# Kernel optimization log

Hardware: AMD Instinct MI355X
Metric: run time of the kernel (lower is better)

Reference implementation:

```python
import jax, jax.numpy as jnp
import numpy as np
from functools import partial

B, F, H, G, S = 8192, 16, 128, 4, 20  # batch, features, hidden, goals, SUBSTEPS
A_IZH, B_IZH, C_IZH, D_IZH = 0.02, 0.2, -65.0, 8.0  # Izhikevich 'RS' params
RATE_DECAY = 0.9
GAMMA, LR = 0.95, 1e-3


def izh_step(v, u, rate, I):
    """One Izhikevich substep (dt=1): returns new (v, u, rate, spike)."""
    v_new = v + (0.04 * v * v + 5.0 * v + 140.0 - u + I)
    u_new = u + A_IZH * (B_IZH * v - u)
    spike = (v_new >= 30.0).astype(v.dtype)
    v_new = jnp.where(spike > 0, C_IZH, v_new)
    u_new = u_new + spike * D_IZH
    rate_new = RATE_DECAY * rate + (1.0 - RATE_DECAY) * spike
    return v_new, u_new, rate_new, spike


def build_features(energy, threat, food_visible, goal, cls_probs, DA_, NA_):
    # [B,16] = [4 scalars | one-hot goal (4) | cls_probs (5) | DA | NA | hunger]
    base = jnp.stack([energy / 100.0, threat, food_visible, 1.0 - energy / 100.0], axis=-1)
    onehot = jax.nn.one_hot(goal, G, dtype=base.dtype)
    tail = jnp.stack([DA_, NA_, jnp.maximum(0.0, 0.5 - energy / 100.0)], axis=-1)
    return jnp.concatenate([base, onehot, cls_probs, tail], axis=-1)


def setup_inputs() -> dict:
    key = jax.random.key(0)
    ks = jax.random.split(key, 16)
    energy = jax.random.uniform(ks[0], (B,)) * 100.0
    threat = jax.random.uniform(ks[1], (B,))
    food_visible = jax.random.uniform(ks[2], (B,))
    goal = jax.random.randint(ks[3], (B,), 0, G)
    prev_goal = jax.random.randint(ks[4], (B,), 0, G)
    DA_ = jax.random.uniform(ks[5], (B,))
    NA_ = jax.random.uniform(ks[6], (B,))
    reward = jax.random.normal(ks[7], (B,)) * 0.5
    cls_probs = jax.nn.softmax(jax.random.normal(ks[8], (B, 5)), axis=-1)
    a_in = 0.5 * np.sqrt(6.0 / (F + H))   # xavier_uniform gain 0.5
    a_out = 0.3 * np.sqrt(6.0 / (H + G))  # xavier_uniform gain 0.3
    W_in_w = jax.random.uniform(ks[9], (B, H, F), minval=-a_in, maxval=a_in)
    W_in_b = jax.random.uniform(ks[10], (B, H), minval=-1.0, maxval=1.0) / np.sqrt(F)
    W_out_w = jax.random.uniform(ks[11], (B, G, H), minval=-a_out, maxval=a_out)
    W_out_b = jax.random.uniform(ks[12], (B, G), minval=-1.0, maxval=1.0) / np.sqrt(H)
    hv = jnp.full((B, H), -65.0)
    hu = B_IZH * hv
    hrate = jnp.zeros((B, H))
    vv = jnp.full((B, G), -65.0)
    vu = B_IZH * vv
    vrate = jnp.zeros((B, G))
    elig_in = jnp.zeros((B, H, F))
    elig_out = jnp.zeros((B, G, H))
    prev_values = jnp.zeros((B, G))
    prev_features = jax.random.uniform(ks[13], (B, F))
    noise = jax.random.normal(ks[14], (S, B, H))
    return dict(energy=energy, threat=threat, food_visible=food_visible, goal=goal,
                prev_goal=prev_goal, DA_=DA_, NA_=NA_, reward=reward, cls_probs=cls_probs,
                W_in_w=W_in_w, W_in_b=W_in_b, W_out_w=W_out_w, W_out_b=W_out_b,
                hv=hv, hu=hu, hrate=hrate, vv=vv, vu=vu, vrate=vrate,
                elig_in=elig_in, elig_out=elig_out, prev_values=prev_values,
                prev_features=prev_features, noise=noise)


def reference(energy, threat, food_visible, goal, prev_goal, DA_, NA_, reward, cls_probs,
              W_in_w, W_in_b, W_out_w, W_out_b, hv, hu, hrate, vv, vu, vrate,
              elig_in, elig_out, prev_values, prev_features, noise):
    features = build_features(energy, threat, food_visible, goal, cls_probs, DA_, NA_)  # [B,F]
    I_in = jnp.einsum('bhf,bf->bh', W_in_w, features) + W_in_b
    I_in = I_in * (5.0 / (jnp.mean(jnp.abs(I_in), axis=-1, keepdims=True) + 1e-8))

    def step(carry, nz):
        hv, hu, hrate, vv, vu, vrate, hsp, vsp = carry
        hv, hu, hrate, sp_h = izh_step(hv, hu, hrate, I_in + 0.3 * nz)
        I_out = jnp.einsum('bgh,bh->bg', W_out_w, hrate) + W_out_b
        I_out = I_out * (4.0 / (jnp.mean(jnp.abs(I_out), axis=-1, keepdims=True) + 1e-8))
        vv, vu, vrate, sp_v = izh_step(vv, vu, vrate, I_out)
        return (hv, hu, hrate, vv, vu, vrate, hsp + sp_h, vsp + sp_v), None

    carry0 = (hv, hu, hrate, vv, vu, vrate, jnp.zeros_like(hrate), jnp.zeros_like(vrate))
    (hv, hu, hrate, vv, vu, vrate, h_spikes, v_spikes), _ = jax.lax.scan(step, carry0, noise)

    values = jnp.einsum('bgh,bh->bg', W_out_w, hrate) + W_out_b  # [B,G]
    V_now = jnp.take_along_axis(values, goal[:, None], axis=1)[:, 0]
    V_prev = jnp.take_along_axis(prev_values, prev_goal[:, None], axis=1)[:, 0]
    td = reward + GAMMA * V_now - V_prev  # [B]

    elig_in_new = 0.9 * elig_in + hrate[:, :, None] * prev_features[:, None, :]
    elig_out_new = 0.9 * elig_out + vrate[:, :, None] * hrate[:, None, :]

    upd = (jnp.abs(td) > 1e-3)  # [B]
    scale = (LR * td * DA_)[:, None, None]
    W_in_new = jnp.where(upd[:, None, None], jnp.clip(W_in_w + scale * elig_in_new, -3.0, 3.0), W_in_w)
    W_out_new = jnp.where(upd[:, None, None], jnp.clip(W_out_w + scale * elig_out_new, -3.0, 3.0), W_out_w)

    hidden_active = jnp.mean((h_spikes > 0).astype(values.dtype), axis=-1)  # [B]
    return values, td, hidden_active, W_in_new, W_out_new, elig_in_new, elig_out_new
```

## Files before the change

### kernel.cpp

```cpp
#include <hip/hip_runtime.h>


namespace {

constexpr int F = 16;
constexpr int H = 128;
constexpr int G = 4;
constexpr int S = 20;

__device__ __forceinline__ float clip3(float x) {
    return fminf(fmaxf(x, -3.0f), 3.0f);
}

__global__ __launch_bounds__(128)
void spiking_critic_kernel(
    const float* __restrict__ energy,
    const float* __restrict__ threat,
    const float* __restrict__ food_visible,
    const int*   __restrict__ goal,
    const int*   __restrict__ prev_goal,
    const float* __restrict__ DA,
    const float* __restrict__ NA,
    const float* __restrict__ reward,
    const float* __restrict__ cls_probs,
    const float* __restrict__ W_in_w,
    const float* __restrict__ W_in_b,
    const float* __restrict__ W_out_w,
    const float* __restrict__ W_out_b,
    const float* __restrict__ hv_in,
    const float* __restrict__ hu_in,
    const float* __restrict__ hrate_in,
    const float* __restrict__ vv_in,
    const float* __restrict__ vu_in,
    const float* __restrict__ vrate_in,
    const float* __restrict__ elig_in,
    const float* __restrict__ elig_out,
    const float* __restrict__ prev_values,
    const float* __restrict__ prev_features,
    const float* __restrict__ noise,
    float* __restrict__ out_values,
    float* __restrict__ out_td,
    float* __restrict__ out_hidden,
    float* __restrict__ out_Win,
    float* __restrict__ out_Wout,
    float* __restrict__ out_ein,
    float* __restrict__ out_eout,
    int nB)
{
    const int b = blockIdx.x;
    const int t = threadIdx.x;

    __shared__ float w_in_lds[H * F];
    __shared__ float w_out_lds[G * H];
    __shared__ float feat[F];
    __shared__ float pf_lds[F];
    __shared__ float hrate_lds[H];
    __shared__ float wob[G];
    __shared__ float iout_lds[G];
    __shared__ float vals_lds[G];
    __shared__ float vrate_lds[G];
    __shared__ float red[2];
    __shared__ float tdsh;

    const float4* wi4 = (const float4*)(W_in_w + (size_t)b * (H * F));
    float4* wl4 = (float4*)w_in_lds;
    #pragma unroll
    for (int k = 0; k < 4; ++k) wl4[t + 128 * k] = wi4[t + 128 * k];
    ((float4*)w_out_lds)[t] = ((const float4*)(W_out_w + (size_t)b * (G * H)))[t];

    if (t < F) pf_lds[t] = prev_features[(size_t)b * F + t];
    if (t < G) wob[t]    = W_out_b[(size_t)b * G + t];

    if (t < F) {
        float e = energy[b];
        float v;
        if      (t == 0)  v = e / 100.0f;
        else if (t == 1)  v = threat[b];
        else if (t == 2)  v = food_visible[b];
        else if (t == 3)  v = 1.0f - e / 100.0f;
        else if (t < 8)   v = (goal[b] == (t - 4)) ? 1.0f : 0.0f;
        else if (t < 13)  v = cls_probs[(size_t)b * 5 + (t - 8)];
        else if (t == 13) v = DA[b];
        else if (t == 14) v = NA[b];
        else              v = fmaxf(0.0f, 0.5f - e / 100.0f);
        feat[t] = v;
    }
    __syncthreads();

    float dot = 0.0f;
    #pragma unroll
    for (int j = 0; j < 4; ++j) {
        float4 w = ((const float4*)w_in_lds)[t * 4 + j];
        dot += w.x * feat[4 * j + 0] + w.y * feat[4 * j + 1]
             + w.z * feat[4 * j + 2] + w.w * feat[4 * j + 3];
    }
    float Iraw = dot + W_in_b[(size_t)b * H + t];
    float a = fabsf(Iraw);
    #pragma unroll
    for (int m = 32; m >= 1; m >>= 1) a += __shfl_xor(a, m, 64);
    if ((t & 63) == 0) red[t >> 6] = a;
    __syncthreads();
    float meanI = (red[0] + red[1]) * (1.0f / 128.0f);
    float Iin = Iraw * (5.0f / (meanI + 1e-8f));

    float hv = hv_in[(size_t)b * H + t];
    float hu = hu_in[(size_t)b * H + t];
    float hr = hrate_in[(size_t)b * H + t];
    float hsp = 0.0f;
    float vvv = 0.0f, vuu = 0.0f, vrr = 0.0f;
    if (t < G) {
        vvv = vv_in[(size_t)b * G + t];
        vuu = vu_in[(size_t)b * G + t];
        vrr = vrate_in[(size_t)b * G + t];
    }

    float nz[S];
    #pragma unroll
    for (int s = 0; s < S; ++s)
        nz[s] = noise[((size_t)s * nB + b) * H + t];

    const int g = t >> 5;
    const int l = t & 31;

    #pragma unroll
    for (int s = 0; s < S; ++s) {
        float I  = Iin + 0.3f * nz[s];
        float vn = hv + (0.04f * hv * hv + 5.0f * hv + 140.0f - hu + I);
        float un = hu + 0.02f * (0.2f * hv - hu);
        float sp = (vn >= 30.0f) ? 1.0f : 0.0f;
        hv = (sp > 0.0f) ? -65.0f : vn;
        hu = un + sp * 8.0f;
        hr = 0.9f * hr + 0.1f * sp;
        hsp += sp;
        hrate_lds[t] = hr;
        __syncthreads();

        float p = 0.0f;
        #pragma unroll
        for (int k = 0; k < 4; ++k) {
            int h = l + 32 * k;
            p += w_out_lds[g * H + h] * hrate_lds[h];
        }
        #pragma unroll
        for (int m = 16; m >= 1; m >>= 1) p += __shfl_xor(p, m, 64);
        if (l == 0) iout_lds[g] = p + wob[g];
        __syncthreads();

        if (t < G) {
            float m4 = 0.25f * (fabsf(iout_lds[0]) + fabsf(iout_lds[1])
                              + fabsf(iout_lds[2]) + fabsf(iout_lds[3]));
            float Io  = iout_lds[t] * (4.0f / (m4 + 1e-8f));
            float vn2 = vvv + (0.04f * vvv * vvv + 5.0f * vvv + 140.0f - vuu + Io);
            float un2 = vuu + 0.02f * (0.2f * vvv - vuu);
            float spv = (vn2 >= 30.0f) ? 1.0f : 0.0f;
            vvv = (spv > 0.0f) ? -65.0f : vn2;
            vuu = un2 + spv * 8.0f;
            vrr = 0.9f * vrr + 0.1f * spv;
        }
    }

    if (t < G) vrate_lds[t] = vrr;
    float p = 0.0f;
    #pragma unroll
    for (int k = 0; k < 4; ++k) {
        int h = l + 32 * k;
        p += w_out_lds[g * H + h] * hrate_lds[h];
    }
    #pragma unroll
    for (int m = 16; m >= 1; m >>= 1) p += __shfl_xor(p, m, 64);
    if (l == 0) {
        float val = p + wob[g];
        vals_lds[g] = val;
        out_values[(size_t)b * G + g] = val;
    }

    unsigned long long mb = __ballot(hsp > 0.0f);
    if ((t & 63) == 0) red[t >> 6] = (float)__popcll(mb);
    __syncthreads();

    if (t == 0) {
        float Vnow  = vals_lds[goal[b]];
        float Vprev = prev_values[(size_t)b * G + prev_goal[b]];
        float td = reward[b] + 0.95f * Vnow - Vprev;
        out_td[b]     = td;
        out_hidden[b] = (red[0] + red[1]) * (1.0f / 128.0f);
        tdsh = td;
    }
    __syncthreads();

    const float td    = tdsh;
    const float scale = 1e-3f * td * DA[b];
    const bool  upd   = fabsf(td) > 1e-3f;

    {
        const float4* ei4 = (const float4*)(elig_in + (size_t)b * (H * F));
        float4* oW = (float4*)(out_Win + (size_t)b * (H * F));
        float4* oE = (float4*)(out_ein + (size_t)b * (H * F));
        const float4* pf4 = (const float4*)pf_lds;
        #pragma unroll
        for (int k = 0; k < 4; ++k) {
            int q = t + 128 * k;
            int h = q >> 2;
            int j = q & 3;
            float4 e  = ei4[q];
            float4 pf = pf4[j];
            float  hrv = hrate_lds[h];
            float4 en;
            en.x = 0.9f * e.x + hrv * pf.x;
            en.y = 0.9f * e.y + hrv * pf.y;
            en.z = 0.9f * e.z + hrv * pf.z;
            en.w = 0.9f * e.w + hrv * pf.w;
            oE[q] = en;
            float4 w = wl4[q];
            float4 wn;
            if (upd) {
                wn.x = clip3(w.x + scale * en.x);
                wn.y = clip3(w.y + scale * en.y);
                wn.z = clip3(w.z + scale * en.z);
                wn.w = clip3(w.w + scale * en.w);
            } else {
                wn = w;
            }
            oW[q] = wn;
        }
    }

    {
        const float4* eo4 = (const float4*)(elig_out + (size_t)b * (G * H));
        float4* oW = (float4*)(out_Wout + (size_t)b * (G * H));
        float4* oE = (float4*)(out_eout + (size_t)b * (G * H));
        int q  = t;
        int gg = q >> 5;
        int h0 = (q & 31) * 4;
        float4 e  = eo4[q];
        float  vrv = vrate_lds[gg];
        float4 en;
        en.x = 0.9f * e.x + vrv * hrate_lds[h0 + 0];
        en.y = 0.9f * e.y + vrv * hrate_lds[h0 + 1];
        en.z = 0.9f * e.z + vrv * hrate_lds[h0 + 2];
        en.w = 0.9f * e.w + vrv * hrate_lds[h0 + 3];
        oE[q] = en;
        float4 w = ((const float4*)w_out_lds)[q];
        float4 wn;
        if (upd) {
            wn.x = clip3(w.x + scale * en.x);
            wn.y = clip3(w.y + scale * en.y);
            wn.z = clip3(w.z + scale * en.z);
            wn.w = clip3(w.w + scale * en.w);
        } else {
            wn = w;
        }
        oW[q] = wn;
    }
}

}

extern "C" void kernel_launch(void* const* d_in, const int* in_sizes, int n_in,
                              void* d_out, int out_size, void* d_ws, size_t ws_size,
                              hipStream_t stream) {
    const int nB = in_sizes[0];

    float* out        = (float*)d_out;
    float* out_values = out;
    float* out_td     = out_values + (size_t)nB * G;
    float* out_hidden = out_td + nB;
    float* out_Win    = out_hidden + nB;
    float* out_Wout   = out_Win + (size_t)nB * H * F;
    float* out_ein    = out_Wout + (size_t)nB * G * H;
    float* out_eout   = out_ein + (size_t)nB * H * F;

    spiking_critic_kernel<<<dim3(nB), dim3(128), 0, stream>>>(
        (const float*)d_in[0],  (const float*)d_in[1],  (const float*)d_in[2],
        (const int*)  d_in[3],  (const int*)  d_in[4],
        (const float*)d_in[5],  (const float*)d_in[6],  (const float*)d_in[7],
        (const float*)d_in[8],  (const float*)d_in[9],  (const float*)d_in[10],
        (const float*)d_in[11], (const float*)d_in[12], (const float*)d_in[13],
        (const float*)d_in[14], (const float*)d_in[15], (const float*)d_in[16],
        (const float*)d_in[17], (const float*)d_in[18], (const float*)d_in[19],
        (const float*)d_in[20], (const float*)d_in[21], (const float*)d_in[22],
        (const float*)d_in[23],
        out_values, out_td, out_hidden, out_Win, out_Wout, out_ein, out_eout,
        nB);
}
```

Baseline: 394.5 us.

## Use one wavefront per batch row and drop per-substep block barriers

The kernel now runs each batch element with a single 64-thread wavefront, each thread owning two hidden neurons. The per-substep output projection is done with register-held W_out columns and wave-wide shuffle reductions, and every thread redundantly integrates the four value neurons. This removes the two __syncthreads and LDS round-trips per substep and the serial t<G branch. The trade-off is more registers per thread (two noise arrays, duplicated value state) and half as many threads per block, which may lower latency hiding for the memory-heavy update phase.

```diff
diff --git a/kernel.cpp b/kernel.cpp
--- a/kernel.cpp
+++ b/kernel.cpp
@@ -12,7 +12,7 @@
     return fminf(fmaxf(x, -3.0f), 3.0f);
 }
 
-__global__ __launch_bounds__(128)
+__global__ __launch_bounds__(64)
 void spiking_critic_kernel(
     const float* __restrict__ energy,
     const float* __restrict__ threat,
@@ -50,26 +50,22 @@
     const int b = blockIdx.x;
     const int t = threadIdx.x;
 
-    __shared__ float w_in_lds[H * F];
-    __shared__ float w_out_lds[G * H];
-    __shared__ float feat[F];
-    __shared__ float pf_lds[F];
-    __shared__ float hrate_lds[H];
-    __shared__ float wob[G];
-    __shared__ float iout_lds[G];
-    __shared__ float vals_lds[G];
-    __shared__ float vrate_lds[G];
-    __shared__ float red[2];
-    __shared__ float tdsh;
+    __shared__ __align__(16) float w_in_lds[H * F];
+    __shared__ __align__(16) float w_out_lds[G * H];
+    __shared__ __align__(16) float hrate_lds[H];
+    __shared__ __align__(16) float feat[F];
+    __shared__ __align__(16) float pf_lds[F];
 
     const float4* wi4 = (const float4*)(W_in_w + (size_t)b * (H * F));
     float4* wl4 = (float4*)w_in_lds;
     #pragma unroll
-    for (int k = 0; k < 4; ++k) wl4[t + 128 * k] = wi4[t + 128 * k];
-    ((float4*)w_out_lds)[t] = ((const float4*)(W_out_w + (size_t)b * (G * H)))[t];
+    for (int k = 0; k < 8; ++k) wl4[t + 64 * k] = wi4[t + 64 * k];
+    const float4* wog = (const float4*)(W_out_w + (size_t)b * (G * H));
+    float4* wo4 = (float4*)w_out_lds;
+    #pragma unroll
+    for (int k = 0; k < 2; ++k) wo4[t + 64 * k] = wog[t + 64 * k];
 
     if (t < F) pf_lds[t] = prev_features[(size_t)b * F + t];
-    if (t < G) wob[t]    = W_out_b[(size_t)b * G + t];
 
     if (t < F) {
         float e = energy[b];
@@ -87,108 +83,129 @@
     }
     __syncthreads();
 
-    float dot = 0.0f;
+    float Iraw0 = W_in_b[(size_t)b * H + t];
+    float Iraw1 = W_in_b[(size_t)b * H + t + 64];
     #pragma unroll
     for (int j = 0; j < 4; ++j) {
-        float4 w = ((const float4*)w_in_lds)[t * 4 + j];
-        dot += w.x * feat[4 * j + 0] + w.y * feat[4 * j + 1]
-             + w.z * feat[4 * j + 2] + w.w * feat[4 * j + 3];
-    }
-    float Iraw = dot + W_in_b[(size_t)b * H + t];
-    float a = fabsf(Iraw);
+        float4 w0 = ((const float4*)w_in_lds)[t * 4 + j];
+        float4 w1 = ((const float4*)w_in_lds)[(t + 64) * 4 + j];
+        float fx = feat[4 * j + 0], fy = feat[4 * j + 1];
+        float fz = feat[4 * j + 2], fw = feat[4 * j + 3];
+        Iraw0 += w0.x * fx + w0.y * fy + w0.z * fz + w0.w * fw;
+        Iraw1 += w1.x * fx + w1.y * fy + w1.z * fz + w1.w * fw;
+    }
+    float a = fabsf(Iraw0) + fabsf(Iraw1);
     #pragma unroll
     for (int m = 32; m >= 1; m >>= 1) a += __shfl_xor(a, m, 64);
-    if ((t & 63) == 0) red[t >> 6] = a;
+    float inorm = 5.0f / (a * (1.0f / 128.0f) + 1e-8f);
+    float Iin0 = Iraw0 * inorm;
+    float Iin1 = Iraw1 * inorm;
+
+    float wc0[G], wc1[G], wob[G];
+    #pragma unroll
+    for (int g = 0; g < G; ++g) {
+        wc0[g] = w_out_lds[g * H + t];
+        wc1[g] = w_out_lds[g * H + t + 64];
+        wob[g] = W_out_b[(size_t)b * G + g];
+    }
+
+    float hv0 = hv_in[(size_t)b * H + t],      hv1 = hv_in[(size_t)b * H + t + 64];
+    float hu0 = hu_in[(size_t)b * H + t],      hu1 = hu_in[(size_t)b * H + t + 64];
+    float hr0 = hrate_in[(size_t)b * H + t],   hr1 = hrate_in[(size_t)b * H + t + 64];
+    float vv[G], vu[G], vr[G];
+    #pragma unroll
+    for (int g = 0; g < G; ++g) {
+        vv[g] = vv_in[(size_t)b * G + g];
+        vu[g] = vu_in[(size_t)b * G + g];
+        vr[g] = vrate_in[(size_t)b * G + g];
+    }
+
+    float nz0[S], nz1[S];
+    #pragma unroll
+    for (int s = 0; s < S; ++s) {
+        nz0[s] = noise[((size_t)s * nB + b) * H + t];
+        nz1[s] = noise[((size_t)s * nB + b) * H + t + 64];
+    }
+
+    float hsp0 = 0.0f, hsp1 = 0.0f;
+    float vals[G] = {0.f, 0.f, 0.f, 0.f};
+
+    #pragma unroll
+    for (int s = 0; s < S; ++s) {
+        {
+            float I  = Iin0 + 0.3f * nz0[s];
+            float vn = hv0 + (0.04f * hv0 * hv0 + 5.0f * hv0 + 140.0f - hu0 + I);
+            float un = hu0 + 0.02f * (0.2f * hv0 - hu0);
+            float sp = (vn >= 30.0f) ? 1.0f : 0.0f;
+            hv0 = (sp > 0.0f) ? -65.0f : vn;
+            hu0 = un + sp * 8.0f;
+            hr0 = 0.9f * hr0 + 0.1f * sp;
+            hsp0 += sp;
+        }
+        {
+            float I  = Iin1 + 0.3f * nz1[s];
+            float vn = hv1 + (0.04f * hv1 * hv1 + 5.0f * hv1 + 140.0f - hu1 + I);
+            float un = hu1 + 0.02f * (0.2f * hv1 - hu1);
+            float sp = (vn >= 30.0f) ? 1.0f : 0.0f;
+            hv1 = (sp > 0.0f) ? -65.0f : vn;
+            hu1 = un + sp * 8.0f;
+            hr1 = 0.9f * hr1 + 0.1f * sp;
+            hsp1 += sp;
+        }
+
+        float p0 = wc0[0] * hr0 + wc1[0] * hr1;
+        float p1 = wc0[1] * hr0 + wc1[1] * hr1;
+        float p2 = wc0[2] * hr0 + wc1[2] * hr1;
+        float p3 = wc0[3] * hr0 + wc1[3] * hr1;
+        #pragma unroll
+        for (int m = 32; m >= 1; m >>= 1) {
+            p0 += __shfl_xor(p0, m, 64);
+            p1 += __shfl_xor(p1, m, 64);
+            p2 += __shfl_xor(p2, m, 64);
+            p3 += __shfl_xor(p3, m, 64);
+        }
+        vals[0] = p0 + wob[0];
+        vals[1] = p1 + wob[1];
+        vals[2] = p2 + wob[2];
+        vals[3] = p3 + wob[3];
+
+        float m4 = 0.25f * (fabsf(vals[0]) + fabsf(vals[1])
+                          + fabsf(vals[2]) + fabsf(vals[3]));
+        float onorm = 4.0f / (m4 + 1e-8f);
+        #pragma unroll
+        for (int g = 0; g < G; ++g) {
+            float Io = vals[g] * onorm;
+            float vn = vv[g] + (0.04f * vv[g] * vv[g] + 5.0f * vv[g] + 140.0f - vu[g] + Io);
+            float un = vu[g] + 0.02f * (0.2f * vv[g] - vu[g]);
+            float sp = (vn >= 30.0f) ? 1.0f : 0.0f;
+            vv[g] = (sp > 0.0f) ? -65.0f : vn;
+            vu[g] = un + sp * 8.0f;
+            vr[g] = 0.9f * vr[g] + 0.1f * sp;
+        }
+    }
+
+    hrate_lds[t] = hr0;
+    hrate_lds[t + 64] = hr1;
     __syncthreads();
-    float meanI = (red[0] + red[1]) * (1.0f / 128.0f);
-    float Iin = Iraw * (5.0f / (meanI + 1e-8f));
-
-    float hv = hv_in[(size_t)b * H + t];
-    float hu = hu_in[(size_t)b * H + t];
-    float hr = hrate_in[(size_t)b * H + t];
-    float hsp = 0.0f;
-    float vvv = 0.0f, vuu = 0.0f, vrr = 0.0f;
+
     if (t < G) {
-        vvv = vv_in[(size_t)b * G + t];
-        vuu = vu_in[(size_t)b * G + t];
-        vrr = vrate_in[(size_t)b * G + t];
-    }
-
-    float nz[S];
-    #pragma unroll
-    for (int s = 0; s < S; ++s)
-        nz[s] = noise[((size_t)s * nB + b) * H + t];
-
-    const int g = t >> 5;
-    const int l = t & 31;
-
-    #pragma unroll
-    for (int s = 0; s < S; ++s) {
-        float I  = Iin + 0.3f * nz[s];
-        float vn = hv + (0.04f * hv * hv + 5.0f * hv + 140.0f - hu + I);
-        float un = hu + 0.02f * (0.2f * hv - hu);
-        float sp = (vn >= 30.0f) ? 1.0f : 0.0f;
-        hv = (sp > 0.0f) ? -65.0f : vn;
-        hu = un + sp * 8.0f;
-        hr = 0.9f * hr + 0.1f * sp;
-        hsp += sp;
-        hrate_lds[t] = hr;
-        __syncthreads();
-
-        float p = 0.0f;
-        #pragma unroll
-        for (int k = 0; k < 4; ++k) {
-            int h = l + 32 * k;
-            p += w_out_lds[g * H + h] * hrate_lds[h];
-        }
-        #pragma unroll
-        for (int m = 16; m >= 1; m >>= 1) p += __shfl_xor(p, m, 64);
-        if (l == 0) iout_lds[g] = p + wob[g];
-        __syncthreads();
-
-        if (t < G) {
-            float m4 = 0.25f * (fabsf(iout_lds[0]) + fabsf(iout_lds[1])
-                              + fabsf(iout_lds[2]) + fabsf(iout_lds[3]));
-            float Io  = iout_lds[t] * (4.0f / (m4 + 1e-8f));
-            float vn2 = vvv + (0.04f * vvv * vvv + 5.0f * vvv + 140.0f - vuu + Io);
-            float un2 = vuu + 0.02f * (0.2f * vvv - vuu);
-            float spv = (vn2 >= 30.0f) ? 1.0f : 0.0f;
-            vvv = (spv > 0.0f) ? -65.0f : vn2;
-            vuu = un2 + spv * 8.0f;
-            vrr = 0.9f * vrr + 0.1f * spv;
-        }
-    }
-
-    if (t < G) vrate_lds[t] = vrr;
-    float p = 0.0f;
-    #pragma unroll
-    for (int k = 0; k < 4; ++k) {
-        int h = l + 32 * k;
-        p += w_out_lds[g * H + h] * hrate_lds[h];
-    }
-    #pragma unroll
-    for (int m = 16; m >= 1; m >>= 1) p += __shfl_xor(p, m, 64);
-    if (l == 0) {
-        float val = p + wob[g];
-        vals_lds[g] = val;
-        out_values[(size_t)b * G + g] = val;
-    }
-
-    unsigned long long mb = __ballot(hsp > 0.0f);
-    if ((t & 63) == 0) red[t >> 6] = (float)__popcll(mb);
-    __syncthreads();
-
+        float v = (t == 0) ? vals[0] : (t == 1) ? vals[1] : (t == 2) ? vals[2] : vals[3];
+        out_values[(size_t)b * G + t] = v;
+    }
+
+    unsigned long long mb0 = __ballot(hsp0 > 0.0f);
+    unsigned long long mb1 = __ballot(hsp1 > 0.0f);
+    float hidden = (float)(__popcll(mb0) + __popcll(mb1)) * (1.0f / 128.0f);
+
+    int gl = goal[b];
+    float Vnow  = (gl == 0) ? vals[0] : (gl == 1) ? vals[1] : (gl == 2) ? vals[2] : vals[3];
+    float Vprev = prev_values[(size_t)b * G + prev_goal[b]];
+    float td = reward[b] + 0.95f * Vnow - Vprev;
     if (t == 0) {
-        float Vnow  = vals_lds[goal[b]];
-        float Vprev = prev_values[(size_t)b * G + prev_goal[b]];
-        float td = reward[b] + 0.95f * Vnow - Vprev;
         out_td[b]     = td;
-        out_hidden[b] = (red[0] + red[1]) * (1.0f / 128.0f);
-        tdsh = td;
-    }
-    __syncthreads();
-
-    const float td    = tdsh;
+        out_hidden[b] = hidden;
+    }
+
     const float scale = 1e-3f * td * DA[b];
     const bool  upd   = fabsf(td) > 1e-3f;
 
@@ -196,15 +213,12 @@
         const float4* ei4 = (const float4*)(elig_in + (size_t)b * (H * F));
         float4* oW = (float4*)(out_Win + (size_t)b * (H * F));
         float4* oE = (float4*)(out_ein + (size_t)b * (H * F));
-        const float4* pf4 = (const float4*)pf_lds;
+        float4 pf = ((const float4*)pf_lds)[t & 3];
         #pragma unroll
-        for (int k = 0; k < 4; ++k) {
-            int q = t + 128 * k;
-            int h = q >> 2;
-            int j = q & 3;
+        for (int k = 0; k < 8; ++k) {
+            int q = t + 64 * k;
             float4 e  = ei4[q];
-            float4 pf = pf4[j];
-            float  hrv = hrate_lds[h];
+            float  hrv = hrate_lds[q >> 2];
             float4 en;
             en.x = 0.9f * e.x + hrv * pf.x;
             en.y = 0.9f * e.y + hrv * pf.y;
@@ -229,28 +243,31 @@
         const float4* eo4 = (const float4*)(elig_out + (size_t)b * (G * H));
         float4* oW = (float4*)(out_Wout + (size_t)b * (G * H));
         float4* oE = (float4*)(out_eout + (size_t)b * (G * H));
-        int q  = t;
-        int gg = q >> 5;
-        int h0 = (q & 31) * 4;
-        float4 e  = eo4[q];
-        float  vrv = vrate_lds[gg];
-        float4 en;
-        en.x = 0.9f * e.x + vrv * hrate_lds[h0 + 0];
-        en.y = 0.9f * e.y + vrv * hrate_lds[h0 + 1];
-        en.z = 0.9f * e.z + vrv * hrate_lds[h0 + 2];
-        en.w = 0.9f * e.w + vrv * hrate_lds[h0 + 3];
-        oE[q] = en;
-        float4 w = ((const float4*)w_out_lds)[q];
-        float4 wn;
-        if (upd) {
-            wn.x = clip3(w.x + scale * en.x);
-            wn.y = clip3(w.y + scale * en.y);
-            wn.z = clip3(w.z + scale * en.z);
-            wn.w = clip3(w.w + scale * en.w);
-        } else {
-            wn = w;
-        }
-        oW[q] = wn;
+        #pragma unroll
+        for (int k = 0; k < 2; ++k) {
+            int q  = t + 64 * k;
+            int gg = q >> 5;
+            float vrv = (gg == 0) ? vr[0] : (gg == 1) ? vr[1] : (gg == 2) ? vr[2] : vr[3];
+            float4 hq = ((const float4*)hrate_lds)[q & 31];
+            float4 e  = eo4[q];
+            float4 en;
+            en.x = 0.9f * e.x + vrv * hq.x;
+            en.y = 0.9f * e.y + vrv * hq.y;
+            en.z = 0.9f * e.z + vrv * hq.z;
+            en.w = 0.9f * e.w + vrv * hq.w;
+            oE[q] = en;
+            float4 w = ((const float4*)w_out_lds)[q];
+            float4 wn;
+            if (upd) {
+                wn.x = clip3(w.x + scale * en.x);
+                wn.y = clip3(w.y + scale * en.y);
+                wn.z = clip3(w.z + scale * en.z);
+                wn.w = clip3(w.w + scale * en.w);
+            } else {
+                wn = w;
+            }
+            oW[q] = wn;
+        }
     }
 }
 
@@ -270,7 +287,7 @@
     float* out_ein    = out_Wout + (size_t)nB * G * H;
     float* out_eout   = out_ein + (size_t)nB * H * F;
 
-    spiking_critic_kernel<<<dim3(nB), dim3(128), 0, stream>>>(
+    spiking_critic_kernel<<<dim3(nB), dim3(64), 0, stream>>>(
         (const float*)d_in[0],  (const float*)d_in[1],  (const float*)d_in[2],
         (const int*)  d_in[3],  (const int*)  d_in[4],
         (const float*)d_in[5],  (const float*)d_in[6],  (const float*)d_in[7],
```

After: 412.5 us. 1.05x slower.
